# Kernel optimization log

Hardware: AMD Instinct MI355X
Metric: run time of the kernel (lower is better)

## Reference

```python
import jax, jax.numpy as jnp
import numpy as np

K_DIM = 128

def setup_inputs() -> dict:
    key = jax.random.key(0)
    k1, k2, k3, k4 = jax.random.split(key, 4)
    B, S, D = 4, 4096, 1024
    input_vec = jax.random.normal(k1, (B, S, D), dtype=jnp.float32)
    # 'normal' Keras initializer ~ RandomNormal(stddev=0.05)
    weight_query = jax.random.normal(k2, (D, K_DIM), dtype=jnp.float32) * 0.05
    weight_key = jax.random.normal(k3, (D, K_DIM), dtype=jnp.float32) * 0.05
    weight_value = jax.random.normal(k4, (D, K_DIM), dtype=jnp.float32) * 0.05
    return {"input_vec": input_vec, "weight_query": weight_query,
            "weight_key": weight_key, "weight_value": weight_value}

def reference(input_vec, weight_query, weight_key, weight_value):
    # Q/K/V projections: [B,S,D] @ [D,K] -> [B,S,K]
    q = jnp.einsum('bsd,dk->bsk', input_vec, weight_query)
    k = jnp.einsum('bsd,dk->bsk', input_vec, weight_key)
    v = jnp.einsum('bsd,dk->bsk', input_vec, weight_value)
    scale = 1.0 / jnp.sqrt(jnp.asarray(K_DIM, dtype=q.dtype))
    # full score matrix [B,S,S], softmax over last axis (keys)
    scores = jnp.einsum('bqk,bsk->bqs', q, k) * scale
    attn = jax.nn.softmax(scores, axis=-1)
    return jnp.einsum('bqs,bsk->bqk', attn, v)
```

## Files before the change

kernel.cpp:

```cpp
#include <hip/hip_runtime.h>
#include <math.h>

#define B_  4
#define S_  4096
#define D_  1024
#define KD_ 128

typedef __attribute__((ext_vector_type(8))) short short8;
typedef __attribute__((ext_vector_type(4))) float f32x4;
typedef __attribute__((ext_vector_type(4))) unsigned short us4;

__device__ __forceinline__ unsigned short f2bf(float f) {
    unsigned int u = __float_as_uint(f);
    u += 0x7fffu + ((u >> 16) & 1u);
    return (unsigned short)(u >> 16);
}

__device__ __forceinline__ f32x4 mfma_bf16(short8 a, short8 b, f32x4 c) {
    return __builtin_amdgcn_mfma_f32_16x16x32_bf16(a, b, c, 0, 0, 0);
}

__device__ __forceinline__ void g2l16(const void* g, void* l) {
    __builtin_amdgcn_global_load_lds(
        (const __attribute__((address_space(1))) unsigned int*)g,
        (__attribute__((address_space(3))) unsigned int*)l, 16, 0, 0);
}

__global__ void convert_w_kernel(const float* __restrict__ wq,
                                 const float* __restrict__ wk,
                                 const float* __restrict__ wv,
                                 unsigned short* __restrict__ wt) {
    int t = blockIdx.x * 256 + threadIdx.x;
    int w = t >> 14;
    int r = t & 16383;
    int n = r & 127;
    int k8 = r >> 7;
    const float* src = (w == 0) ? wq : (w == 1) ? wk : wv;
    float scale = (w == 0) ? 0.12751725551033443f : 1.0f;
    short8 v;
#pragma unroll
    for (int i = 0; i < 8; ++i)
        v[i] = (short)f2bf(src[(size_t)(k8 * 8 + i) * KD_ + n] * scale);
    *reinterpret_cast<short8*>(&wt[(size_t)w * KD_ * D_ + (size_t)n * D_ + k8 * 8]) = v;
}

__global__ __launch_bounds__(256) void proj_kernel(
        const float* __restrict__ X, const unsigned short* __restrict__ Wt,
        unsigned short* __restrict__ Qo, unsigned short* __restrict__ Ko,
        unsigned short* __restrict__ Vt) {
    const int mtile = blockIdx.x;
    const int which = blockIdx.y;
    const int m0 = mtile * 128;
    const int tid = threadIdx.x;
    const int lane = tid & 63;
    const int wid = tid >> 6;
    const int wr = wid >> 1, wc = wid & 1;
    const int l15 = lane & 15, l4 = lane >> 4;

    __shared__ __align__(16) unsigned short Asm[128 * 64];
    __shared__ __align__(16) unsigned short Bsm[128 * 64];
    __shared__ __align__(16) unsigned short Tsm[128 * 128];

    const unsigned short* W = Wt + (size_t)which * KD_ * D_;

    f32x4 acc[4][4];
#pragma unroll
    for (int r = 0; r < 4; ++r)
#pragma unroll
        for (int c = 0; c < 4; ++c) acc[r][c] = (f32x4)0.0f;

    for (int k0 = 0; k0 < D_; k0 += 64) {
#pragma unroll
        for (int i = 0; i < 8; ++i) {
            int f = tid + i * 256;
            int row = f >> 4, c4 = f & 15;
            float4 xv = *reinterpret_cast<const float4*>(
                &X[(size_t)(m0 + row) * D_ + k0 + c4 * 4]);
            us4 h;
            h.x = f2bf(xv.x); h.y = f2bf(xv.y); h.z = f2bf(xv.z); h.w = f2bf(xv.w);
            *reinterpret_cast<us4*>(&Asm[row * 64 + c4 * 4]) = h;
        }
#pragma unroll
        for (int i = 0; i < 4; ++i) {
            int g = tid + i * 256;
            int n = g >> 3, c8 = g & 7;
            *reinterpret_cast<short8*>(&Bsm[n * 64 + c8 * 8]) =
                *reinterpret_cast<const short8*>(&W[(size_t)n * D_ + k0 + c8 * 8]);
        }
        __syncthreads();

        short8 a[4][2], b[4][2];
#pragma unroll
        for (int rt = 0; rt < 4; ++rt)
#pragma unroll
            for (int kc = 0; kc < 2; ++kc)
                a[rt][kc] = *reinterpret_cast<const short8*>(
                    &Asm[(wr * 64 + rt * 16 + l15) * 64 + kc * 32 + l4 * 8]);
#pragma unroll
        for (int ct = 0; ct < 4; ++ct)
#pragma unroll
            for (int kc = 0; kc < 2; ++kc)
                b[ct][kc] = *reinterpret_cast<const short8*>(
                    &Bsm[(wc * 64 + ct * 16 + l15) * 64 + kc * 32 + l4 * 8]);
#pragma unroll
        for (int kc = 0; kc < 2; ++kc)
#pragma unroll
            for (int rt = 0; rt < 4; ++rt)
#pragma unroll
                for (int ct = 0; ct < 4; ++ct)
                    acc[rt][ct] = mfma_bf16(a[rt][kc], b[ct][kc], acc[rt][ct]);
        __syncthreads();
    }

    if (which < 2) {
        unsigned short* O = (which == 0) ? Qo : Ko;
#pragma unroll
        for (int rt = 0; rt < 4; ++rt)
#pragma unroll
            for (int ct = 0; ct < 4; ++ct)
#pragma unroll
                for (int j = 0; j < 4; ++j) {
                    int row = m0 + wr * 64 + rt * 16 + l4 * 4 + j;
                    int col = wc * 64 + ct * 16 + l15;
                    O[(size_t)row * KD_ + col] = f2bf(acc[rt][ct][j]);
                }
    } else {
#pragma unroll
        for (int rt = 0; rt < 4; ++rt)
#pragma unroll
            for (int ct = 0; ct < 4; ++ct)
#pragma unroll
                for (int j = 0; j < 4; ++j) {
                    int row = wr * 64 + rt * 16 + l4 * 4 + j;
                    int col = wc * 64 + ct * 16 + l15;
                    Tsm[col * 128 + row] = f2bf(acc[rt][ct][j]);
                }
        __syncthreads();
        int bb = m0 >> 12;
        int s0 = m0 & 4095;
#pragma unroll
        for (int i = 0; i < 8; ++i) {
            int g = tid + i * 256;
            int n = g >> 4, s8 = g & 15;
            *reinterpret_cast<short8*>(
                &Vt[(size_t)bb * KD_ * S_ + (size_t)n * S_ + s0 + s8 * 8]) =
                *reinterpret_cast<short8*>(&Tsm[n * 128 + s8 * 8]);
        }
    }
}

__global__ __launch_bounds__(512) void attn_kernel(
        const unsigned short* __restrict__ Q,
        const unsigned short* __restrict__ Kb,
        const unsigned short* __restrict__ Vt,
        float* __restrict__ Out) {
    const int qt = blockIdx.x;
    const int b = blockIdx.y;
    const int tid = threadIdx.x;
    const int lane = tid & 63;
    const int wid = tid >> 6;
    const int grp = wid >> 2;
    const int wg  = wid & 3;
    const int q0 = qt * 64;
    const int l15 = lane & 15, l4 = lane >> 4;

    __shared__ __align__(16) unsigned short Ksm[2][2][64 * 128];
    __shared__ __align__(16) unsigned short Vsm[2][2][128 * 64];
    __shared__ __align__(16) unsigned short Psm[8][16 * 64];

    short8 aq[4];
    {
        const unsigned short* qrow =
            Q + ((size_t)(b * S_ + q0 + wg * 16 + l15)) * KD_;
#pragma unroll
        for (int kc = 0; kc < 4; ++kc)
            aq[kc] = *reinterpret_cast<const short8*>(&qrow[kc * 32 + l4 * 8]);
    }

    f32x4 acc[8];
#pragma unroll
    for (int i = 0; i < 8; ++i) acc[i] = (f32x4)0.0f;
    float lsum[4] = {0.0f, 0.0f, 0.0f, 0.0f};

    const unsigned short* Kbase = Kb + (size_t)b * S_ * KD_;
    const unsigned short* Vbase = Vt + (size_t)b * KD_ * S_;

    auto STAGE = [&](int buf, int kt) {
#pragma unroll
        for (int i = 0; i < 4; ++i) {
            int d = i * 256 + wg * 64 + lane;
            int row = d >> 4, c = d & 15;
            g2l16(&Kbase[(size_t)(kt * 64 + row) * KD_ + (size_t)((c ^ (row & 7)) * 8)],
                  &Ksm[grp][buf][(i * 256 + wg * 64) * 8]);
        }
#pragma unroll
        for (int i = 0; i < 4; ++i) {
            int d = i * 256 + wg * 64 + lane;
            int row = d >> 3, c = d & 7;
            g2l16(&Vbase[(size_t)row * S_ + kt * 64 + (c ^ (row & 7)) * 8],
                  &Vsm[grp][buf][(i * 256 + wg * 64) * 8]);
        }
    };

    int cur = 0;
    STAGE(0, grp);
    __syncthreads();

    for (int it = 0; it < 32; ++it) {
        if (it < 31) STAGE(cur ^ 1, (it + 1) * 2 + grp);

        const unsigned short* ksm = &Ksm[grp][cur][0];
        const unsigned short* vsm = &Vsm[grp][cur][0];

        f32x4 sf[4];
#pragma unroll
        for (int ct = 0; ct < 4; ++ct) sf[ct] = (f32x4)0.0f;
        __builtin_amdgcn_s_setprio(1);
#pragma unroll
        for (int kc = 0; kc < 4; ++kc)
#pragma unroll
            for (int ct = 0; ct < 4; ++ct) {
                int row = ct * 16 + l15;
                int e = (kc * 32 + l4 * 8) ^ ((row & 7) << 3);
                short8 bk = *reinterpret_cast<const short8*>(&ksm[row * 128 + e]);
                sf[ct] = mfma_bf16(aq[kc], bk, sf[ct]);
            }
        __builtin_amdgcn_s_setprio(0);

#pragma unroll
        for (int ct = 0; ct < 4; ++ct)
#pragma unroll
            for (int j = 0; j < 4; ++j) {
                float p = exp2f(sf[ct][j]);
                sf[ct][j] = p;
                lsum[j] += p;
            }

#pragma unroll
        for (int ct = 0; ct < 4; ++ct)
#pragma unroll
            for (int j = 0; j < 4; ++j) {
                int row = l4 * 4 + j;
                int col = (ct * 16 + l15) ^ ((row & 7) << 3);
                Psm[wid][row * 64 + col] = f2bf(sf[ct][j]);
            }

        __builtin_amdgcn_s_setprio(1);
#pragma unroll
        for (int kc = 0; kc < 2; ++kc) {
            int eP = (kc * 32 + l4 * 8) ^ ((l15 & 7) << 3);
            short8 pa = *reinterpret_cast<const short8*>(&Psm[wid][l15 * 64 + eP]);
#pragma unroll
            for (int c8 = 0; c8 < 8; ++c8) {
                int row = c8 * 16 + l15;
                int eV = (kc * 32 + l4 * 8) ^ ((row & 7) << 3);
                short8 bv = *reinterpret_cast<const short8*>(&vsm[row * 64 + eV]);
                acc[c8] = mfma_bf16(pa, bv, acc[c8]);
            }
        }
        __builtin_amdgcn_s_setprio(0);
        __syncthreads();
        cur ^= 1;
    }

#pragma unroll
    for (int j = 0; j < 4; ++j) {
        float t = lsum[j];
        t += __shfl_xor(t, 1);
        t += __shfl_xor(t, 2);
        t += __shfl_xor(t, 4);
        t += __shfl_xor(t, 8);
        lsum[j] = t;
    }

    float* accS = (float*)&Ksm[0][0][0];
    float* mlS  = (float*)&Vsm[0][0][0];
    if (grp == 1) {
#pragma unroll
        for (int c8 = 0; c8 < 8; ++c8)
#pragma unroll
            for (int j = 0; j < 4; ++j)
                accS[(wg * 16 + l4 * 4 + j) * 128 + c8 * 16 + l15] = acc[c8][j];
        if (l15 == 0) {
#pragma unroll
            for (int j = 0; j < 4; ++j)
                mlS[wg * 16 + l4 * 4 + j] = lsum[j];
        }
    }
    __syncthreads();
    if (grp == 0) {
        float* Ob = Out + (size_t)b * S_ * KD_;
#pragma unroll
        for (int j = 0; j < 4; ++j) {
            int rw = wg * 16 + l4 * 4 + j;
            float inv = 1.0f / (lsum[j] + mlS[rw]);
#pragma unroll
            for (int c8 = 0; c8 < 8; ++c8) {
                float o = (acc[c8][j] + accS[rw * 128 + c8 * 16 + l15]) * inv;
                Ob[(size_t)(q0 + rw) * KD_ + c8 * 16 + l15] = o;
            }
        }
    }
}

extern "C" void kernel_launch(void* const* d_in, const int* in_sizes, int n_in,
                              void* d_out, int out_size, void* d_ws, size_t ws_size,
                              hipStream_t stream) {
    const float* X  = (const float*)d_in[0];
    const float* Wq = (const float*)d_in[1];
    const float* Wk = (const float*)d_in[2];
    const float* Wv = (const float*)d_in[3];
    float* Out = (float*)d_out;

    unsigned short* Wt  = (unsigned short*)d_ws;
    unsigned short* Q16 = (unsigned short*)((char*)d_ws + 786432);
    unsigned short* K16 = Q16 + (size_t)16384 * 128;
    unsigned short* V16 = K16 + (size_t)16384 * 128;

    hipLaunchKernelGGL(convert_w_kernel, dim3(192), dim3(256), 0, stream,
                       Wq, Wk, Wv, Wt);
    hipLaunchKernelGGL(proj_kernel, dim3(128, 3), dim3(256), 0, stream,
                       X, Wt, Q16, K16, V16);
    hipLaunchKernelGGL(attn_kernel, dim3(64, 4), dim3(512), 0, stream,
                       Q16, K16, V16, Out);
}
```

Measured before the change: 116.0 us.

## Split attention keys into four wave groups with 32-row tiles and register reuse

The attention kernel now splits the key sequence across four wave groups of two waves each instead of two groups of four. Each wave computes 32 query rows, so every K and V fragment read from LDS feeds two MFMAs. Key tiles shrink to 32 rows with a new V swizzle, and the epilogue reduces partial outputs and row sums from three groups through a 144KB LDS scratch buffer. The aim is fewer LDS reads per MFMA and more parallelism over keys. The cost is higher register pressure, a larger end-of-kernel reduction, and bf16 conversion switched to the library intrinsic.

Result: faster. 97.39 us (-16.1%).

```diff
diff --git a/kernel.cpp b/kernel.cpp
--- a/kernel.cpp
+++ b/kernel.cpp
@@ -1,4 +1,5 @@
 #include <hip/hip_runtime.h>
+#include <hip/hip_bf16.h>
 #include <math.h>
 
 #define B_  4
@@ -11,9 +12,8 @@
 typedef __attribute__((ext_vector_type(4))) unsigned short us4;
 
 __device__ __forceinline__ unsigned short f2bf(float f) {
-    unsigned int u = __float_as_uint(f);
-    u += 0x7fffu + ((u >> 16) & 1u);
-    return (unsigned short)(u >> 16);
+    __hip_bfloat16 h = __float2bfloat16(f);
+    return *reinterpret_cast<unsigned short*>(&h);
 }
 
 __device__ __forceinline__ f32x4 mfma_bf16(short8 a, short8 b, f32x4 c) {
@@ -149,7 +149,7 @@
     }
 }
 
-__global__ __launch_bounds__(512) void attn_kernel(
+__global__ __launch_bounds__(512, 2) void attn_kernel(
         const unsigned short* __restrict__ Q,
         const unsigned short* __restrict__ Kb,
         const unsigned short* __restrict__ Vt,
@@ -159,46 +159,55 @@
     const int tid = threadIdx.x;
     const int lane = tid & 63;
     const int wid = tid >> 6;
-    const int grp = wid >> 2;
-    const int wg  = wid & 3;
+    const int grp = wid >> 1;
+    const int wg  = wid & 1;
     const int q0 = qt * 64;
     const int l15 = lane & 15, l4 = lane >> 4;
 
-    __shared__ __align__(16) unsigned short Ksm[2][2][64 * 128];
-    __shared__ __align__(16) unsigned short Vsm[2][2][128 * 64];
-    __shared__ __align__(16) unsigned short Psm[8][16 * 64];
-
-    short8 aq[4];
+    __shared__ __align__(16) unsigned char lds_raw[147456];
+    unsigned short* KsmA = (unsigned short*)lds_raw;
+    unsigned short* VsmA = (unsigned short*)(lds_raw + 65536);
+    unsigned short* Psm  = (unsigned short*)(lds_raw + 131072);
+
+    short8 aq[2][4];
     {
-        const unsigned short* qrow =
-            Q + ((size_t)(b * S_ + q0 + wg * 16 + l15)) * KD_;
-#pragma unroll
-        for (int kc = 0; kc < 4; ++kc)
-            aq[kc] = *reinterpret_cast<const short8*>(&qrow[kc * 32 + l4 * 8]);
-    }
-
-    f32x4 acc[8];
-#pragma unroll
-    for (int i = 0; i < 8; ++i) acc[i] = (f32x4)0.0f;
-    float lsum[4] = {0.0f, 0.0f, 0.0f, 0.0f};
+#pragma unroll
+        for (int a = 0; a < 2; ++a) {
+            const unsigned short* qrow =
+                Q + ((size_t)(b * S_ + q0 + wg * 32 + a * 16 + l15)) * KD_;
+#pragma unroll
+            for (int kc = 0; kc < 4; ++kc)
+                aq[a][kc] = *reinterpret_cast<const short8*>(&qrow[kc * 32 + l4 * 8]);
+        }
+    }
+
+    f32x4 acc[2][8];
+#pragma unroll
+    for (int a = 0; a < 2; ++a)
+#pragma unroll
+        for (int i = 0; i < 8; ++i) acc[a][i] = (f32x4)0.0f;
+    float lsum[2][4] = {{0,0,0,0},{0,0,0,0}};
 
     const unsigned short* Kbase = Kb + (size_t)b * S_ * KD_;
     const unsigned short* Vbase = Vt + (size_t)b * KD_ * S_;
 
+    unsigned short* Kgrp = KsmA + grp * 2 * 4096;
+    unsigned short* Vgrp = VsmA + grp * 2 * 4096;
+
     auto STAGE = [&](int buf, int kt) {
 #pragma unroll
         for (int i = 0; i < 4; ++i) {
-            int d = i * 256 + wg * 64 + lane;
+            int d = i * 128 + wg * 64 + lane;
             int row = d >> 4, c = d & 15;
-            g2l16(&Kbase[(size_t)(kt * 64 + row) * KD_ + (size_t)((c ^ (row & 7)) * 8)],
-                  &Ksm[grp][buf][(i * 256 + wg * 64) * 8]);
+            g2l16(&Kbase[(size_t)(kt * 32 + row) * KD_ + ((c ^ (row & 7)) * 8)],
+                  &Kgrp[(buf * 512 + i * 128 + wg * 64) * 8]);
         }
 #pragma unroll
         for (int i = 0; i < 4; ++i) {
-            int d = i * 256 + wg * 64 + lane;
-            int row = d >> 3, c = d & 7;
-            g2l16(&Vbase[(size_t)row * S_ + kt * 64 + (c ^ (row & 7)) * 8],
-                  &Vsm[grp][buf][(i * 256 + wg * 64) * 8]);
+            int d = i * 128 + wg * 64 + lane;
+            int row = d >> 2, c = d & 3;
+            g2l16(&Vbase[(size_t)row * S_ + kt * 32 + ((c ^ ((row >> 1) & 3)) * 8)],
+                  &Vgrp[(buf * 512 + i * 128 + wg * 64) * 8]);
         }
     };
 
@@ -207,56 +216,59 @@
     __syncthreads();
 
     for (int it = 0; it < 32; ++it) {
-        if (it < 31) STAGE(cur ^ 1, (it + 1) * 2 + grp);
-
-        const unsigned short* ksm = &Ksm[grp][cur][0];
-        const unsigned short* vsm = &Vsm[grp][cur][0];
-
-        f32x4 sf[4];
-#pragma unroll
-        for (int ct = 0; ct < 4; ++ct) sf[ct] = (f32x4)0.0f;
+        if (it < 31) STAGE(cur ^ 1, (it + 1) * 4 + grp);
+
+        const unsigned short* ksm = Kgrp + cur * 4096;
+        const unsigned short* vsm = Vgrp + cur * 4096;
+
+        f32x4 sf[2][2];
+#pragma unroll
+        for (int a = 0; a < 2; ++a)
+#pragma unroll
+            for (int ct = 0; ct < 2; ++ct) sf[a][ct] = (f32x4)0.0f;
         __builtin_amdgcn_s_setprio(1);
 #pragma unroll
         for (int kc = 0; kc < 4; ++kc)
 #pragma unroll
-            for (int ct = 0; ct < 4; ++ct) {
+            for (int ct = 0; ct < 2; ++ct) {
                 int row = ct * 16 + l15;
-                int e = (kc * 32 + l4 * 8) ^ ((row & 7) << 3);
-                short8 bk = *reinterpret_cast<const short8*>(&ksm[row * 128 + e]);
-                sf[ct] = mfma_bf16(aq[kc], bk, sf[ct]);
+                short8 bk = *reinterpret_cast<const short8*>(
+                    &ksm[row * 128 + (((kc * 4 + l4) ^ (row & 7)) * 8)]);
+#pragma unroll
+                for (int a = 0; a < 2; ++a)
+                    sf[a][ct] = mfma_bf16(aq[a][kc], bk, sf[a][ct]);
             }
         __builtin_amdgcn_s_setprio(0);
 
 #pragma unroll
-        for (int ct = 0; ct < 4; ++ct)
-#pragma unroll
-            for (int j = 0; j < 4; ++j) {
-                float p = exp2f(sf[ct][j]);
-                sf[ct][j] = p;
-                lsum[j] += p;
-            }
-
-#pragma unroll
-        for (int ct = 0; ct < 4; ++ct)
-#pragma unroll
-            for (int j = 0; j < 4; ++j) {
-                int row = l4 * 4 + j;
-                int col = (ct * 16 + l15) ^ ((row & 7) << 3);
-                Psm[wid][row * 64 + col] = f2bf(sf[ct][j]);
-            }
+        for (int a = 0; a < 2; ++a)
+#pragma unroll
+            for (int ct = 0; ct < 2; ++ct)
+#pragma unroll
+                for (int j = 0; j < 4; ++j) {
+                    float p = exp2f(sf[a][ct][j]);
+                    lsum[a][j] += p;
+                    int r = a * 16 + l4 * 4 + j;
+                    int cswz = ((ct * 2 + (l15 >> 3)) ^ ((r >> 1) & 3)) * 8 + (l15 & 7);
+                    Psm[wid * 1024 + r * 32 + cswz] = f2bf(p);
+                }
 
         __builtin_amdgcn_s_setprio(1);
-#pragma unroll
-        for (int kc = 0; kc < 2; ++kc) {
-            int eP = (kc * 32 + l4 * 8) ^ ((l15 & 7) << 3);
-            short8 pa = *reinterpret_cast<const short8*>(&Psm[wid][l15 * 64 + eP]);
-#pragma unroll
-            for (int c8 = 0; c8 < 8; ++c8) {
-                int row = c8 * 16 + l15;
-                int eV = (kc * 32 + l4 * 8) ^ ((row & 7) << 3);
-                short8 bv = *reinterpret_cast<const short8*>(&vsm[row * 64 + eV]);
-                acc[c8] = mfma_bf16(pa, bv, acc[c8]);
-            }
+        short8 pa[2];
+#pragma unroll
+        for (int a = 0; a < 2; ++a) {
+            int r = a * 16 + l15;
+            pa[a] = *reinterpret_cast<const short8*>(
+                &Psm[wid * 1024 + r * 32 + ((l4 ^ ((r >> 1) & 3)) * 8)]);
+        }
+#pragma unroll
+        for (int c8 = 0; c8 < 8; ++c8) {
+            int row = c8 * 16 + l15;
+            short8 bv = *reinterpret_cast<const short8*>(
+                &vsm[row * 32 + ((l4 ^ ((row >> 1) & 3)) * 8)]);
+#pragma unroll
+            for (int a = 0; a < 2; ++a)
+                acc[a][c8] = mfma_bf16(pa[a], bv, acc[a][c8]);
         }
         __builtin_amdgcn_s_setprio(0);
         __syncthreads();
@@ -264,42 +276,51 @@
     }
 
 #pragma unroll
-    for (int j = 0; j < 4; ++j) {
-        float t = lsum[j];
-        t += __shfl_xor(t, 1);
-        t += __shfl_xor(t, 2);
-        t += __shfl_xor(t, 4);
-        t += __shfl_xor(t, 8);
-        lsum[j] = t;
-    }
-
-    float* accS = (float*)&Ksm[0][0][0];
-    float* mlS  = (float*)&Vsm[0][0][0];
-    if (grp == 1) {
-#pragma unroll
-        for (int c8 = 0; c8 < 8; ++c8)
-#pragma unroll
-            for (int j = 0; j < 4; ++j)
-                accS[(wg * 16 + l4 * 4 + j) * 128 + c8 * 16 + l15] = acc[c8][j];
-        if (l15 == 0) {
-#pragma unroll
-            for (int j = 0; j < 4; ++j)
-                mlS[wg * 16 + l4 * 4 + j] = lsum[j];
-        }
+    for (int a = 0; a < 2; ++a)
+#pragma unroll
+        for (int j = 0; j < 4; ++j) {
+            float t = lsum[a][j];
+            t += __shfl_xor(t, 1);
+            t += __shfl_xor(t, 2);
+            t += __shfl_xor(t, 4);
+            t += __shfl_xor(t, 8);
+            lsum[a][j] = t;
+        }
+
+    float* scratch = (float*)lds_raw;
+    float* lsumS   = (float*)(lds_raw + 98304);
+    __syncthreads();
+    if (grp >= 1) {
+        int base = (grp - 1) * 8192;
+#pragma unroll
+        for (int a = 0; a < 2; ++a)
+#pragma unroll
+            for (int j = 0; j < 4; ++j) {
+                int row = wg * 32 + a * 16 + l4 * 4 + j;
+#pragma unroll
+                for (int c8 = 0; c8 < 8; ++c8)
+                    scratch[base + row * 128 + c8 * 16 + l15] = acc[a][c8][j];
+                if (l15 == 0) lsumS[(grp - 1) * 64 + row] = lsum[a][j];
+            }
     }
     __syncthreads();
     if (grp == 0) {
         float* Ob = Out + (size_t)b * S_ * KD_;
 #pragma unroll
-        for (int j = 0; j < 4; ++j) {
-            int rw = wg * 16 + l4 * 4 + j;
-            float inv = 1.0f / (lsum[j] + mlS[rw]);
-#pragma unroll
-            for (int c8 = 0; c8 < 8; ++c8) {
-                float o = (acc[c8][j] + accS[rw * 128 + c8 * 16 + l15]) * inv;
-                Ob[(size_t)(q0 + rw) * KD_ + c8 * 16 + l15] = o;
+        for (int a = 0; a < 2; ++a)
+#pragma unroll
+            for (int j = 0; j < 4; ++j) {
+                int row = wg * 32 + a * 16 + l4 * 4 + j;
+                float l = lsum[a][j] + lsumS[row] + lsumS[64 + row] + lsumS[128 + row];
+                float inv = 1.0f / l;
+#pragma unroll
+                for (int c8 = 0; c8 < 8; ++c8) {
+                    int idx = row * 128 + c8 * 16 + l15;
+                    float o = acc[a][c8][j] + scratch[idx] + scratch[8192 + idx] +
+                              scratch[16384 + idx];
+                    Ob[(size_t)(q0 + row) * KD_ + c8 * 16 + l15] = o * inv;
+                }
             }
-        }
     }
 }
 
```
